# Optimization experiments

Hardware: AMD Instinct MI355X
Metric: run time of the kernel (lower is better)

The kernel has to match this reference:

```python
import jax, jax.numpy as jnp
import numpy as np

N = 50000      # nodes
E = 800000     # edges
F_IN = 512     # num_features
H = 128        # hidden


def setup_inputs() -> dict:
    key = jax.random.key(0)
    ks = jax.random.split(key, 10)
    edge_index = jax.random.randint(ks[0], (2, E), 0, N, dtype=jnp.int64 if jax.config.jax_enable_x64 else jnp.int32)
    x = jax.random.normal(ks[1], (N, F_IN), jnp.float32)
    weights = jax.random.uniform(ks[2], (E,), jnp.float32)
    def w(i, shape, fan):
        return jax.random.normal(ks[i], shape, jnp.float32) / np.sqrt(fan).astype(np.float32)
    return {
        "edge_index": edge_index,
        "x": x,
        "weights": weights,
        "W_lin1": w(3, (F_IN, H), F_IN), "b_lin1": jnp.zeros((H,), jnp.float32),
        "W_conv1": w(4, (H, 2 * H), H), "b_conv1": jnp.zeros((2 * H,), jnp.float32),
        "W_mu": w(5, (2 * H, H), 2 * H), "b_mu": jnp.zeros((H,), jnp.float32),
        "W_lin": w(6, (2 * H, 1), 2 * H), "b_lin": jnp.zeros((1,), jnp.float32),
    }


def gcn_conv(x, W, b, src, dst, ew, n):
    """PyG GCNConv with edge weights: add self-loops (weight 1), symmetric norm, scatter-add."""
    loop = jnp.arange(n, dtype=src.dtype)
    s2 = jnp.concatenate([src, loop])
    d2 = jnp.concatenate([dst, loop])
    w2 = jnp.concatenate([ew, jnp.ones((n,), x.dtype)])
    deg = jax.ops.segment_sum(w2, d2, num_segments=n)          # weighted in-degree incl. self-loop
    dinv = jnp.where(deg > 0, deg, 1.0) ** -0.5
    dinv = jnp.where(deg > 0, dinv, 0.0)
    norm = dinv[s2] * w2 * dinv[d2]                            # [E+N]
    h = x @ W                                                   # [N, out]
    out = jax.ops.segment_sum(h[s2] * norm[:, None], d2, num_segments=n)
    return out + b


def reference(edge_index, x, weights, W_lin1, b_lin1, W_conv1, b_conv1, W_mu, b_mu, W_lin, b_lin):
    n = x.shape[0]
    src, dst = edge_index[0], edge_index[1]
    # eval mode: dropout is identity, VGAE.encode returns mu
    h = x @ W_lin1 + b_lin1                                     # lin1
    h = jax.nn.relu(gcn_conv(h, W_conv1, b_conv1, src, dst, weights, n))
    z = gcn_conv(h, W_mu, b_mu, src, dst, weights, n)           # mu == embeddings
    emb_edges = jnp.concatenate([z[src], z[dst]], axis=1)       # [E, 2H]
    out = jax.nn.sigmoid(emb_edges @ W_lin + b_lin)
    return out.squeeze(-1)                                      # [E]
```

## Files before the change

kernel.cpp:

```cpp
#include <hip/hip_runtime.h>
#include <hip/hip_bf16.h>
#include <math.h>


#define NSL 256
#define RSH 8
#define RNG 256

typedef __attribute__((ext_vector_type(8))) short bf16x8;
typedef __attribute__((ext_vector_type(4))) float f32x4;

typedef const __attribute__((address_space(1))) unsigned int* gas_t;
typedef __attribute__((address_space(3))) unsigned int* las_t;

static __device__ __forceinline__ void gload_lds16(const void* g, void* l) {
    __builtin_amdgcn_global_load_lds((gas_t)g, (las_t)l, 16, 0, 0);
}

static __device__ __forceinline__ ushort f2b(float f) {
    __hip_bfloat16 h = __float2bfloat16(f);
    return *(ushort*)&h;
}
static __device__ __forceinline__ float b2f(ushort u) {
    unsigned int v = ((unsigned int)u) << 16;
    return *(float*)&v;
}
static __device__ __forceinline__ bf16x8 cvt8(float4 a, float4 b) {
    bf16x8 r;
    r[0] = (short)f2b(a.x); r[1] = (short)f2b(a.y); r[2] = (short)f2b(a.z); r[3] = (short)f2b(a.w);
    r[4] = (short)f2b(b.x); r[5] = (short)f2b(b.y); r[6] = (short)f2b(b.z); r[7] = (short)f2b(b.w);
    return r;
}


__global__ __launch_bounds__(256) void bucket_count(const int* __restrict__ dst,
                                                    int* __restrict__ cntA, int E, int NR) {
    __shared__ int lc[256];
    const int b = blockIdx.x, t = threadIdx.x;
    lc[t] = 0;
    __syncthreads();
    const int beg = (int)((long long)b * E / NSL);
    const int end = (int)((long long)(b + 1) * E / NSL);
    for (int e = beg + t; e < end; e += 256) atomicAdd(&lc[dst[e] >> RSH], 1);
    __syncthreads();
    if (t < NR) cntA[b * NR + t] = lc[t];
}

__global__ __launch_bounds__(256) void range_scan(int* __restrict__ cntA,
                                                  int* __restrict__ rtot, int NR) {
    __shared__ int s_[256];
    const int r = blockIdx.x, t = threadIdx.x;
    int v = cntA[t * NR + r];
    s_[t] = v;
    __syncthreads();
    for (int off = 1; off < 256; off <<= 1) {
        int add = (t >= off) ? s_[t - off] : 0;
        __syncthreads();
        s_[t] += add;
        __syncthreads();
    }
    cntA[t * NR + r] = s_[t] - v;
    if (t == 255) rtot[r] = s_[t];
}

__global__ __launch_bounds__(256) void base_scan(const int* __restrict__ rtot,
                                                 int* __restrict__ baseOut, int NR) {
    __shared__ int s_[256];
    const int t = threadIdx.x;
    int v = (t < NR) ? rtot[t] : 0;
    s_[t] = v;
    __syncthreads();
    for (int off = 1; off < 256; off <<= 1) {
        int add = (t >= off) ? s_[t - off] : 0;
        __syncthreads();
        s_[t] += add;
        __syncthreads();
    }
    if (t < NR) baseOut[t] = s_[t] - v;
    if (t == NR - 1) baseOut[NR] = s_[t];
}

__global__ __launch_bounds__(256) void bucket_scatter(const int* __restrict__ src,
                                                      const int* __restrict__ dst,
                                                      const float* __restrict__ w,
                                                      const int* __restrict__ cntA,
                                                      const int* __restrict__ baseOut,
                                                      unsigned int* __restrict__ packB,
                                                      float* __restrict__ wB, int E, int NR) {
    __shared__ int cur[256];
    const int b = blockIdx.x, t = threadIdx.x;
    if (t < NR) cur[t] = cntA[b * NR + t] + baseOut[t];
    __syncthreads();
    const int beg = (int)((long long)b * E / NSL);
    const int end = (int)((long long)(b + 1) * E / NSL);
    for (int e = beg + t; e < end; e += 256) {
        int d = dst[e];
        int r = d >> RSH;
        int pos = atomicAdd(&cur[r], 1);
        packB[pos] = ((unsigned int)(d & (RNG - 1)) << 24) | (unsigned int)src[e];
        wB[pos] = w[e];
    }
}

__global__ __launch_bounds__(256) void range_deg(const unsigned int* __restrict__ packB,
                                                 const float* __restrict__ wB,
                                                 const int* __restrict__ baseOut,
                                                 float* __restrict__ dinv,
                                                 int* __restrict__ offs,
                                                 int N, int E) {
    __shared__ float lw[256];
    __shared__ int lc[256];
    __shared__ int sc[256];
    const int r = blockIdx.x, t = threadIdx.x;
    lw[t] = 0.f; lc[t] = 0;
    __syncthreads();
    const int beg = baseOut[r], end = baseOut[r + 1];
    for (int e = beg + t; e < end; e += 256) {
        unsigned int pk = packB[e];
        int dl = pk >> 24;
        atomicAdd(&lc[dl], 1);
        atomicAdd(&lw[dl], wB[e]);
    }
    __syncthreads();
    int v = lc[t];
    sc[t] = v;
    __syncthreads();
    for (int off = 1; off < 256; off <<= 1) {
        int add = (t >= off) ? sc[t - off] : 0;
        __syncthreads();
        sc[t] += add;
        __syncthreads();
    }
    int node = (r << RSH) + t;
    if (node < N) {
        dinv[node] = 1.0f / sqrtf(1.0f + lw[t]);
        offs[node] = beg + sc[t] - v;
    }
    if (r == 0 && t == 0) offs[N] = E;
}

__global__ __launch_bounds__(256) void csr_build(const unsigned int* __restrict__ packB,
                                                 const float* __restrict__ wB,
                                                 const int* __restrict__ baseOut,
                                                 const float* __restrict__ dinv,
                                                 const int* __restrict__ offs,
                                                 int* __restrict__ es,
                                                 float* __restrict__ en, int N) {
    __shared__ int cur[256];
    __shared__ float ldv[256];
    const int r = blockIdx.x, t = threadIdx.x;
    const int node = (r << RSH) + t;
    cur[t] = (node < N) ? offs[node] : 0;
    ldv[t] = (node < N) ? dinv[node] : 0.f;
    __syncthreads();
    const int beg = baseOut[r], end = baseOut[r + 1];
    for (int e = beg + t; e < end; e += 256) {
        unsigned int pk = packB[e];
        int dl = pk >> 24;
        int s = pk & 0xFFFFFF;
        float nrm = dinv[s] * wB[e] * ldv[dl];
        int pos = atomicAdd(&cur[dl], 1);
        es[pos] = s;
        en[pos] = nrm;
    }
}


__global__ __launch_bounds__(256) void tconv_kernel(const float* __restrict__ B,
                                                    ushort* __restrict__ BT, int K, int Nn) {
    int i = blockIdx.x * 256 + threadIdx.x;
    if (i < K * Nn) {
        int k = i / Nn, n = i % Nn;
        BT[(size_t)n * K + k] = f2b(B[i]);
    }
}

__global__ __launch_bounds__(256) void fold_kernel(const float* __restrict__ Wm,
                                                   const float* __restrict__ Wl,
                                                   const float* __restrict__ bm,
                                                   float* __restrict__ wmp,
                                                   float* __restrict__ wmq,
                                                   float* __restrict__ bpq) {
    int j = threadIdx.x;
    float sp = 0.f, sq = 0.f;
    for (int k = 0; k < 128; ++k) {
        float v = Wm[(size_t)j * 128 + k];
        sp += v * Wl[k];
        sq += v * Wl[128 + k];
    }
    wmp[j] = sp; wmq[j] = sq;
    if (j == 0) { float s = 0.f; for (int k = 0; k < 128; ++k) s += bm[k] * Wl[k];       bpq[0] = s; }
    if (j == 1) { float s = 0.f; for (int k = 0; k < 128; ++k) s += bm[k] * Wl[128 + k]; bpq[1] = s; }
}

__global__ __launch_bounds__(256) void gemm1_mfma(const float* __restrict__ A,
                                                  const ushort* __restrict__ BT,
                                                  const float* __restrict__ bias,
                                                  ushort* __restrict__ C, int M) {
    __shared__ float  As[64 * 64];
    __shared__ ushort Bs[128 * 64];
    char* AsB = (char*)As;
    char* BsB = (char*)Bs;
    const int t = threadIdx.x;
    const int bm = blockIdx.x * 64;
    const int lane = t & 63;
    const int wid = t >> 6;
    const int wm = (wid >> 1) * 32, wn = (wid & 1) * 64;

    f32x4 acc[2][4] = {};

    const int a_row_l = (lane >> 4);
    const int a_ib    = (lane & 15) * 16;
    const int b_row_l = (lane >> 3);
    const int b_ib    = (lane & 7) * 16;

#pragma unroll 1
    for (int tt = 0; tt < 8; ++tt) {
        const int k0 = tt * 64;
#pragma unroll
        for (int j = 0; j < 4; ++j) {
            int c = wid * 4 + j;
            int row = c * 4 + a_row_l;
            int sw = a_ib ^ ((row & 7) << 5);
            int grow = min(bm + row, M - 1);
            const char* src = (const char*)A + ((size_t)grow * 512 + k0) * 4 + sw;
            gload_lds16(src, AsB + c * 1024);
        }
#pragma unroll
        for (int j = 0; j < 4; ++j) {
            int c = wid * 4 + j;
            int row = c * 8 + b_row_l;
            int sw = b_ib ^ ((row & 7) << 4);
            const char* src = (const char*)BT + (size_t)row * 1024 + k0 * 2 + sw;
            gload_lds16(src, BsB + c * 1024);
        }
        __syncthreads();
#pragma unroll
        for (int ks = 0; ks < 2; ++ks) {
            bf16x8 af[2], bfr[4];
#pragma unroll
            for (int mi = 0; mi < 2; ++mi) {
                int r = wm + mi * 16 + (lane & 15);
                int byte = r * 256 + ks * 128 + (lane >> 4) * 32;
                byte ^= (r & 7) << 5;
                float4 f0 = *(const float4*)(AsB + byte);
                float4 f1 = *(const float4*)(AsB + byte + 16);
                af[mi] = cvt8(f0, f1);
            }
#pragma unroll
            for (int ni = 0; ni < 4; ++ni) {
                int r = wn + ni * 16 + (lane & 15);
                int byte = r * 128 + ks * 64 + (lane >> 4) * 16;
                byte ^= (r & 7) << 4;
                bfr[ni] = *(const bf16x8*)(BsB + byte);
            }
#pragma unroll
            for (int mi = 0; mi < 2; ++mi)
#pragma unroll
                for (int ni = 0; ni < 4; ++ni)
                    acc[mi][ni] = __builtin_amdgcn_mfma_f32_16x16x32_bf16(af[mi], bfr[ni], acc[mi][ni], 0, 0, 0);
        }
        __syncthreads();
    }

#pragma unroll
    for (int ni = 0; ni < 4; ++ni) {
        int col = wn + ni * 16 + (lane & 15);
        float bv = bias[col];
#pragma unroll
        for (int mi = 0; mi < 2; ++mi)
#pragma unroll
            for (int r = 0; r < 4; ++r) {
                int row = bm + wm + mi * 16 + (lane >> 4) * 4 + r;
                if (row < M) C[(size_t)row * 128 + col] = f2b(acc[mi][ni][r] + bv);
            }
    }
}

__global__ __launch_bounds__(256) void aggregate_bf16(const ushort* __restrict__ h,
                                                      const int* __restrict__ offs,
                                                      const int* __restrict__ es,
                                                      const float* __restrict__ en,
                                                      const float* __restrict__ dinv,
                                                      ushort* __restrict__ out, int n) {
    int wave = (int)((blockIdx.x * (size_t)blockDim.x + threadIdx.x) >> 6);
    int lane = threadIdx.x & 63;
    if (wave >= n) return;
    float di = dinv[wave];
    float sw = di * di;
    unsigned int hv = *(const unsigned int*)(h + (size_t)wave * 128 + lane * 2);
    float ax = sw * b2f((ushort)(hv & 0xffff));
    float ay = sw * b2f((ushort)(hv >> 16));
    int beg = offs[wave], end = offs[wave + 1];
    for (int e = beg; e < end; e += 8) {
        int sx[8]; float wx[8];
#pragma unroll
        for (int j = 0; j < 8; ++j) {
            bool v = (e + j) < end;
            sx[j] = v ? es[e + j] : wave;
            wx[j] = v ? en[e + j] : 0.f;
        }
        unsigned int vv[8];
#pragma unroll
        for (int j = 0; j < 8; ++j)
            vv[j] = *(const unsigned int*)(h + (size_t)sx[j] * 128 + lane * 2);
#pragma unroll
        for (int j = 0; j < 8; ++j) {
            ax += wx[j] * b2f((ushort)(vv[j] & 0xffff));
            ay += wx[j] * b2f((ushort)(vv[j] >> 16));
        }
    }
    unsigned int o = (unsigned int)f2b(ax) | ((unsigned int)f2b(ay) << 16);
    *(unsigned int*)(out + (size_t)wave * 128 + lane * 2) = o;
}

__global__ __launch_bounds__(64) void gemm2_stream(const ushort* __restrict__ A,
                                                   const ushort* __restrict__ BT,
                                                   const float* __restrict__ bc,
                                                   const float* __restrict__ wmp,
                                                   const float* __restrict__ wmq,
                                                   float* __restrict__ pe,
                                                   float* __restrict__ qe, int M) {
    const int lane = threadIdx.x;
    const int r0 = blockIdx.x * 16;
    const int lrow = lane & 15;
    const int lk   = (lane >> 4) * 8;

    f32x4 acc[16] = {};

    const ushort* a  = A  + (size_t)min(r0 + lrow, M - 1) * 128 + lk;
    const ushort* bp = BT + (size_t)lrow * 128 + lk;

#pragma unroll
    for (int ks = 0; ks < 4; ++ks) {
        const int k0 = ks * 32;
        bf16x8 af = *(const bf16x8*)(a + k0);
#pragma unroll
        for (int ni = 0; ni < 16; ++ni) {
            bf16x8 bfr = *(const bf16x8*)(bp + (size_t)ni * 16 * 128 + k0);
            acc[ni] = __builtin_amdgcn_mfma_f32_16x16x32_bf16(af, bfr, acc[ni], 0, 0, 0);
        }
    }

    float bcv[16], wpv[16], wqv[16];
#pragma unroll
    for (int ni = 0; ni < 16; ++ni) {
        int col = ni * 16 + lrow;
        bcv[ni] = bc[col];
        wpv[ni] = wmp[col];
        wqv[ni] = wmq[col];
    }
#pragma unroll
    for (int r = 0; r < 4; ++r) {
        float sp = 0.f, sq = 0.f;
#pragma unroll
        for (int ni = 0; ni < 16; ++ni) {
            float h = fmaxf(acc[ni][r] + bcv[ni], 0.f);
            sp += h * wpv[ni];
            sq += h * wqv[ni];
        }
#pragma unroll
        for (int off = 1; off < 16; off <<= 1) {
            sp += __shfl_xor(sp, off);
            sq += __shfl_xor(sq, off);
        }
        if (lrow == 0) {
            int row = r0 + (lane >> 4) * 4 + r;
            if (row < M) { pe[row] = sp; qe[row] = sq; }
        }
    }
}

__global__ __launch_bounds__(256) void agg_scalar(const float* __restrict__ pe,
                                                  const float* __restrict__ qe,
                                                  const int* __restrict__ offs,
                                                  const int* __restrict__ es,
                                                  const float* __restrict__ en,
                                                  const float* __restrict__ dinv,
                                                  const float* __restrict__ bpq,
                                                  float* __restrict__ p,
                                                  float* __restrict__ q, int n) {
    int i = blockIdx.x * 256 + threadIdx.x;
    if (i >= n) return;
    float di = dinv[i];
    float sw = di * di;
    float ap = sw * pe[i], aq = sw * qe[i];
    int beg = offs[i], end = offs[i + 1];
    for (int k = beg; k < end; k += 4) {
        int sx[4]; float wx[4];
#pragma unroll
        for (int j = 0; j < 4; ++j) {
            bool v = (k + j) < end;
            sx[j] = v ? es[k + j] : i;
            wx[j] = v ? en[k + j] : 0.f;
        }
        float pv[4], qv[4];
#pragma unroll
        for (int j = 0; j < 4; ++j) { pv[j] = pe[sx[j]]; qv[j] = qe[sx[j]]; }
#pragma unroll
        for (int j = 0; j < 4; ++j) { ap += wx[j] * pv[j]; aq += wx[j] * qv[j]; }
    }
    p[i] = ap + bpq[0];
    q[i] = aq + bpq[1];
}

__global__ __launch_bounds__(256) void edge_out_kernel(const int* __restrict__ src,
                                                       const int* __restrict__ dst,
                                                       const float* __restrict__ p,
                                                       const float* __restrict__ q,
                                                       const float* __restrict__ bl,
                                                       float* __restrict__ out, int e) {
    int i = blockIdx.x * 256 + threadIdx.x;
    if (i < e) {
        float t = p[src[i]] + q[dst[i]] + bl[0];
        out[i] = 1.0f / (1.0f + expf(-t));
    }
}


extern "C" void kernel_launch(void* const* d_in, const int* in_sizes, int n_in,
                              void* d_out, int out_size, void* d_ws, size_t ws_size,
                              hipStream_t stream) {
    const int*   edge_index = (const int*)d_in[0];
    const float* x   = (const float*)d_in[1];
    const float* w   = (const float*)d_in[2];
    const float* W1  = (const float*)d_in[3];
    const float* b1  = (const float*)d_in[4];
    const float* Wc  = (const float*)d_in[5];
    const float* bc  = (const float*)d_in[6];
    const float* Wm  = (const float*)d_in[7];
    const float* bm  = (const float*)d_in[8];
    const float* Wl  = (const float*)d_in[9];
    const float* bl  = (const float*)d_in[10];
    float* out = (float*)d_out;

    const int E  = in_sizes[2];
    const int H  = in_sizes[4];
    const int F  = in_sizes[3] / H;
    const int N  = in_sizes[1] / F;
    const int H2 = 2 * H;
    const int NR = (N + RNG - 1) / RNG;

    const int* src = edge_index;
    const int* dst = edge_index + E;

    char* ws = (char*)d_ws;
    size_t off = 0;
    auto alloc = [&](size_t bytes) -> void* {
        off = (off + 255) & ~(size_t)255;
        void* r = ws + off;
        off += bytes;
        return r;
    };
    int*          cntA    = (int*)         alloc((size_t)NSL * NR * 4);
    int*          rtot    = (int*)         alloc((size_t)NR * 4);
    int*          baseOut = (int*)         alloc((size_t)(NR + 1) * 4);
    unsigned int* packB   = (unsigned int*)alloc((size_t)E * 4);
    float*        wB      = (float*)       alloc((size_t)E * 4);
    float*        dinv    = (float*)       alloc((size_t)N * 4);
    int*          offs    = (int*)         alloc((size_t)(N + 1) * 4);
    int*          es      = (int*)         alloc((size_t)E * 4);
    float*        en      = (float*)       alloc((size_t)E * 4);
    ushort*       h0_bf   = (ushort*)      alloc((size_t)N * H * 2);
    ushort*       agg1_bf = (ushort*)      alloc((size_t)N * H * 2);
    ushort*       W1T     = (ushort*)      alloc((size_t)H * F * 2);
    ushort*       WcT     = (ushort*)      alloc((size_t)H2 * H * 2);
    float*        wmp     = (float*)       alloc(H2 * 4);
    float*        wmq     = (float*)       alloc(H2 * 4);
    float*        bpq     = (float*)       alloc(2 * 4);
    float*        pe      = (float*)       alloc((size_t)N * 4);
    float*        qe      = (float*)       alloc((size_t)N * 4);
    float*        p       = (float*)       alloc((size_t)N * 4);
    float*        q       = (float*)       alloc((size_t)N * 4);
    (void)ws_size; (void)n_in; (void)out_size;

    int nbN  = (N + 255) / 256;
    int nbE  = (E + 255) / 256;
    int nbW  = (int)(((size_t)N * 64 + 255) / 256);
    int nb64 = (N + 63) / 64;
    int nb16 = (N + 15) / 16;

    bucket_count<<<NSL, 256, 0, stream>>>(dst, cntA, E, NR);
    range_scan<<<NR, 256, 0, stream>>>(cntA, rtot, NR);
    base_scan<<<1, 256, 0, stream>>>(rtot, baseOut, NR);
    bucket_scatter<<<NSL, 256, 0, stream>>>(src, dst, w, cntA, baseOut, packB, wB, E, NR);
    range_deg<<<NR, 256, 0, stream>>>(packB, wB, baseOut, dinv, offs, N, E);
    csr_build<<<NR, 256, 0, stream>>>(packB, wB, baseOut, dinv, offs, es, en, N);

    tconv_kernel<<<(F * H + 255) / 256, 256, 0, stream>>>(W1, W1T, F, H);
    tconv_kernel<<<(H * H2 + 255) / 256, 256, 0, stream>>>(Wc, WcT, H, H2);
    fold_kernel<<<1, 256, 0, stream>>>(Wm, Wl, bm, wmp, wmq, bpq);

    gemm1_mfma<<<nb64, 256, 0, stream>>>(x, W1T, b1, h0_bf, N);
    aggregate_bf16<<<nbW, 256, 0, stream>>>(h0_bf, offs, es, en, dinv, agg1_bf, N);
    gemm2_stream<<<nb16, 64, 0, stream>>>(agg1_bf, WcT, bc, wmp, wmq, pe, qe, N);
    agg_scalar<<<nbN, 256, 0, stream>>>(pe, qe, offs, es, en, dinv, bpq, p, q, N);
    edge_out_kernel<<<nbE, 256, 0, stream>>>(src, dst, p, q, bl, out, E);
}
```

Measured before the change: 184.2 us.

## Fuse degree and CSR build, interleave edge records, prescale by dinv, double-buffer GEMM1

The degree and CSR-build kernels are merged into one range_build kernel. Edge source and weight are packed into interleaved uint2 records, so each edge needs one load instead of two. Symmetric normalization is refactored: dinv is applied to rows in the GEMM epilogue and to destinations after aggregation, so the per-edge dinv[src] gather and multiply go away. GEMM1 now double-buffers its LDS tiles with global_load_lds prefetch and manual vmcnt waits to overlap loads with MFMA, at the cost of twice the LDS per block.

Measured after the change: 197.7 us. +7.3%, slower.

```diff
diff --git a/kernel.cpp b/kernel.cpp
--- a/kernel.cpp
+++ b/kernel.cpp
@@ -85,8 +85,7 @@
                                                       const float* __restrict__ w,
                                                       const int* __restrict__ cntA,
                                                       const int* __restrict__ baseOut,
-                                                      unsigned int* __restrict__ packB,
-                                                      float* __restrict__ wB, int E, int NR) {
+                                                      uint2* __restrict__ rec, int E, int NR) {
     __shared__ int cur[256];
     const int b = blockIdx.x, t = threadIdx.x;
     if (t < NR) cur[t] = cntA[b * NR + t] + baseOut[t];
@@ -97,17 +96,17 @@
         int d = dst[e];
         int r = d >> RSH;
         int pos = atomicAdd(&cur[r], 1);
-        packB[pos] = ((unsigned int)(d & (RNG - 1)) << 24) | (unsigned int)src[e];
-        wB[pos] = w[e];
-    }
-}
-
-__global__ __launch_bounds__(256) void range_deg(const unsigned int* __restrict__ packB,
-                                                 const float* __restrict__ wB,
-                                                 const int* __restrict__ baseOut,
-                                                 float* __restrict__ dinv,
-                                                 int* __restrict__ offs,
-                                                 int N, int E) {
+        rec[pos] = make_uint2(((unsigned int)(d & (RNG - 1)) << 24) | (unsigned int)src[e],
+                              __float_as_uint(w[e]));
+    }
+}
+
+__global__ __launch_bounds__(256) void range_build(const uint2* __restrict__ rec,
+                                                   const int* __restrict__ baseOut,
+                                                   float* __restrict__ dinv,
+                                                   int* __restrict__ offs,
+                                                   uint2* __restrict__ ce,
+                                                   int N, int E) {
     __shared__ float lw[256];
     __shared__ int lc[256];
     __shared__ int sc[256];
@@ -116,10 +115,10 @@
     __syncthreads();
     const int beg = baseOut[r], end = baseOut[r + 1];
     for (int e = beg + t; e < end; e += 256) {
-        unsigned int pk = packB[e];
-        int dl = pk >> 24;
+        uint2 pk = rec[e];
+        int dl = pk.x >> 24;
         atomicAdd(&lc[dl], 1);
-        atomicAdd(&lw[dl], wB[e]);
+        atomicAdd(&lw[dl], __uint_as_float(pk.y));
     }
     __syncthreads();
     int v = lc[t];
@@ -131,37 +130,20 @@
         sc[t] += add;
         __syncthreads();
     }
-    int node = (r << RSH) + t;
+    const int node = (r << RSH) + t;
+    const int o = beg + sc[t] - v;
     if (node < N) {
         dinv[node] = 1.0f / sqrtf(1.0f + lw[t]);
-        offs[node] = beg + sc[t] - v;
+        offs[node] = o;
     }
     if (r == 0 && t == 0) offs[N] = E;
-}
-
-__global__ __launch_bounds__(256) void csr_build(const unsigned int* __restrict__ packB,
-                                                 const float* __restrict__ wB,
-                                                 const int* __restrict__ baseOut,
-                                                 const float* __restrict__ dinv,
-                                                 const int* __restrict__ offs,
-                                                 int* __restrict__ es,
-                                                 float* __restrict__ en, int N) {
-    __shared__ int cur[256];
-    __shared__ float ldv[256];
-    const int r = blockIdx.x, t = threadIdx.x;
-    const int node = (r << RSH) + t;
-    cur[t] = (node < N) ? offs[node] : 0;
-    ldv[t] = (node < N) ? dinv[node] : 0.f;
-    __syncthreads();
-    const int beg = baseOut[r], end = baseOut[r + 1];
+    lc[t] = o;
+    __syncthreads();
     for (int e = beg + t; e < end; e += 256) {
-        unsigned int pk = packB[e];
-        int dl = pk >> 24;
-        int s = pk & 0xFFFFFF;
-        float nrm = dinv[s] * wB[e] * ldv[dl];
-        int pos = atomicAdd(&cur[dl], 1);
-        es[pos] = s;
-        en[pos] = nrm;
+        uint2 pk = rec[e];
+        int dl = pk.x >> 24;
+        int pos = atomicAdd(&lc[dl], 1);
+        ce[pos] = make_uint2(pk.x & 0xFFFFFF, pk.y);
     }
 }
 
@@ -196,11 +178,10 @@
 __global__ __launch_bounds__(256) void gemm1_mfma(const float* __restrict__ A,
                                                   const ushort* __restrict__ BT,
                                                   const float* __restrict__ bias,
+                                                  const float* __restrict__ dinv,
                                                   ushort* __restrict__ C, int M) {
-    __shared__ float  As[64 * 64];
-    __shared__ ushort Bs[128 * 64];
-    char* AsB = (char*)As;
-    char* BsB = (char*)Bs;
+    __shared__ float  As[2][64 * 64];
+    __shared__ ushort Bs[2][128 * 64];
     const int t = threadIdx.x;
     const int bm = blockIdx.x * 64;
     const int lane = t & 63;
@@ -214,9 +195,7 @@
     const int b_row_l = (lane >> 3);
     const int b_ib    = (lane & 7) * 16;
 
-#pragma unroll 1
-    for (int tt = 0; tt < 8; ++tt) {
-        const int k0 = tt * 64;
+    auto stage = [&](int buf, int k0) {
 #pragma unroll
         for (int j = 0; j < 4; ++j) {
             int c = wid * 4 + j;
@@ -224,7 +203,7 @@
             int sw = a_ib ^ ((row & 7) << 5);
             int grow = min(bm + row, M - 1);
             const char* src = (const char*)A + ((size_t)grow * 512 + k0) * 4 + sw;
-            gload_lds16(src, AsB + c * 1024);
+            gload_lds16(src, (char*)As[buf] + c * 1024);
         }
 #pragma unroll
         for (int j = 0; j < 4; ++j) {
@@ -232,9 +211,24 @@
             int row = c * 8 + b_row_l;
             int sw = b_ib ^ ((row & 7) << 4);
             const char* src = (const char*)BT + (size_t)row * 1024 + k0 * 2 + sw;
-            gload_lds16(src, BsB + c * 1024);
-        }
-        __syncthreads();
+            gload_lds16(src, (char*)Bs[buf] + c * 1024);
+        }
+    };
+
+    stage(0, 0);
+    int cur = 0;
+#pragma unroll 1
+    for (int tt = 0; tt < 8; ++tt) {
+        if (tt < 7) {
+            stage(cur ^ 1, (tt + 1) * 64);
+            asm volatile("s_waitcnt vmcnt(8)" ::: "memory");
+        } else {
+            asm volatile("s_waitcnt vmcnt(0)" ::: "memory");
+        }
+        __builtin_amdgcn_sched_barrier(0);
+        __builtin_amdgcn_s_barrier();
+        const char* AsB = (const char*)As[cur];
+        const char* BsB = (const char*)Bs[cur];
 #pragma unroll
         for (int ks = 0; ks < 2; ++ks) {
             bf16x8 af[2], bfr[4];
@@ -260,58 +254,59 @@
                 for (int ni = 0; ni < 4; ++ni)
                     acc[mi][ni] = __builtin_amdgcn_mfma_f32_16x16x32_bf16(af[mi], bfr[ni], acc[mi][ni], 0, 0, 0);
         }
-        __syncthreads();
-    }
-
-#pragma unroll
-    for (int ni = 0; ni < 4; ++ni) {
-        int col = wn + ni * 16 + (lane & 15);
-        float bv = bias[col];
-#pragma unroll
-        for (int mi = 0; mi < 2; ++mi)
-#pragma unroll
-            for (int r = 0; r < 4; ++r) {
-                int row = bm + wm + mi * 16 + (lane >> 4) * 4 + r;
-                if (row < M) C[(size_t)row * 128 + col] = f2b(acc[mi][ni][r] + bv);
+        __builtin_amdgcn_s_barrier();
+        cur ^= 1;
+    }
+
+#pragma unroll
+    for (int mi = 0; mi < 2; ++mi)
+#pragma unroll
+        for (int r = 0; r < 4; ++r) {
+            int row = bm + wm + mi * 16 + (lane >> 4) * 4 + r;
+            if (row < M) {
+                float dv = dinv[row];
+#pragma unroll
+                for (int ni = 0; ni < 4; ++ni) {
+                    int col = wn + ni * 16 + (lane & 15);
+                    C[(size_t)row * 128 + col] = f2b((acc[mi][ni][r] + bias[col]) * dv);
+                }
             }
-    }
-}
-
-__global__ __launch_bounds__(256) void aggregate_bf16(const ushort* __restrict__ h,
+        }
+}
+
+__global__ __launch_bounds__(256) void aggregate_bf16(const ushort* __restrict__ hs,
                                                       const int* __restrict__ offs,
-                                                      const int* __restrict__ es,
-                                                      const float* __restrict__ en,
+                                                      const uint2* __restrict__ ce,
                                                       const float* __restrict__ dinv,
                                                       ushort* __restrict__ out, int n) {
-    int wave = (int)((blockIdx.x * (size_t)blockDim.x + threadIdx.x) >> 6);
+    int node = (int)((blockIdx.x * (size_t)blockDim.x + threadIdx.x) >> 6);
     int lane = threadIdx.x & 63;
-    if (wave >= n) return;
-    float di = dinv[wave];
-    float sw = di * di;
-    unsigned int hv = *(const unsigned int*)(h + (size_t)wave * 128 + lane * 2);
-    float ax = sw * b2f((ushort)(hv & 0xffff));
-    float ay = sw * b2f((ushort)(hv >> 16));
-    int beg = offs[wave], end = offs[wave + 1];
+    if (node >= n) return;
+    unsigned int hv = *(const unsigned int*)(hs + (size_t)node * 128 + lane * 2);
+    float ax = b2f((ushort)(hv & 0xffff));
+    float ay = b2f((ushort)(hv >> 16));
+    int beg = offs[node], end = offs[node + 1];
     for (int e = beg; e < end; e += 8) {
-        int sx[8]; float wx[8];
+        uint2 rr[8];
 #pragma unroll
         for (int j = 0; j < 8; ++j) {
             bool v = (e + j) < end;
-            sx[j] = v ? es[e + j] : wave;
-            wx[j] = v ? en[e + j] : 0.f;
+            rr[j] = v ? ce[e + j] : make_uint2((unsigned)node, 0u);
         }
         unsigned int vv[8];
 #pragma unroll
         for (int j = 0; j < 8; ++j)
-            vv[j] = *(const unsigned int*)(h + (size_t)sx[j] * 128 + lane * 2);
+            vv[j] = *(const unsigned int*)(hs + (size_t)rr[j].x * 128 + lane * 2);
 #pragma unroll
         for (int j = 0; j < 8; ++j) {
-            ax += wx[j] * b2f((ushort)(vv[j] & 0xffff));
-            ay += wx[j] * b2f((ushort)(vv[j] >> 16));
-        }
-    }
-    unsigned int o = (unsigned int)f2b(ax) | ((unsigned int)f2b(ay) << 16);
-    *(unsigned int*)(out + (size_t)wave * 128 + lane * 2) = o;
+            float wj = __uint_as_float(rr[j].y);
+            ax += wj * b2f((ushort)(vv[j] & 0xffff));
+            ay += wj * b2f((ushort)(vv[j] >> 16));
+        }
+    }
+    float dv = dinv[node];
+    unsigned int o = (unsigned int)f2b(ax * dv) | ((unsigned int)f2b(ay * dv) << 16);
+    *(unsigned int*)(out + (size_t)node * 128 + lane * 2) = o;
 }
 
 __global__ __launch_bounds__(64) void gemm2_stream(const ushort* __restrict__ A,
@@ -319,6 +314,7 @@
                                                    const float* __restrict__ bc,
                                                    const float* __restrict__ wmp,
                                                    const float* __restrict__ wmq,
+                                                   const float* __restrict__ dinv,
                                                    float* __restrict__ pe,
                                                    float* __restrict__ qe, int M) {
     const int lane = threadIdx.x;
@@ -366,7 +362,11 @@
         }
         if (lrow == 0) {
             int row = r0 + (lane >> 4) * 4 + r;
-            if (row < M) { pe[row] = sp; qe[row] = sq; }
+            if (row < M) {
+                float dv = dinv[row];
+                pe[row] = sp * dv;
+                qe[row] = sq * dv;
+            }
         }
     }
 }
@@ -374,34 +374,35 @@
 __global__ __launch_bounds__(256) void agg_scalar(const float* __restrict__ pe,
                                                   const float* __restrict__ qe,
                                                   const int* __restrict__ offs,
-                                                  const int* __restrict__ es,
-                                                  const float* __restrict__ en,
+                                                  const uint2* __restrict__ ce,
                                                   const float* __restrict__ dinv,
                                                   const float* __restrict__ bpq,
                                                   float* __restrict__ p,
                                                   float* __restrict__ q, int n) {
     int i = blockIdx.x * 256 + threadIdx.x;
     if (i >= n) return;
-    float di = dinv[i];
-    float sw = di * di;
-    float ap = sw * pe[i], aq = sw * qe[i];
+    float ap = pe[i], aq = qe[i];
     int beg = offs[i], end = offs[i + 1];
     for (int k = beg; k < end; k += 4) {
-        int sx[4]; float wx[4];
+        uint2 rr[4];
 #pragma unroll
         for (int j = 0; j < 4; ++j) {
             bool v = (k + j) < end;
-            sx[j] = v ? es[k + j] : i;
-            wx[j] = v ? en[k + j] : 0.f;
+            rr[j] = v ? ce[k + j] : make_uint2((unsigned)i, 0u);
         }
         float pv[4], qv[4];
 #pragma unroll
-        for (int j = 0; j < 4; ++j) { pv[j] = pe[sx[j]]; qv[j] = qe[sx[j]]; }
-#pragma unroll
-        for (int j = 0; j < 4; ++j) { ap += wx[j] * pv[j]; aq += wx[j] * qv[j]; }
-    }
-    p[i] = ap + bpq[0];
-    q[i] = aq + bpq[1];
+        for (int j = 0; j < 4; ++j) { pv[j] = pe[rr[j].x]; qv[j] = qe[rr[j].x]; }
+#pragma unroll
+        for (int j = 0; j < 4; ++j) {
+            float wj = __uint_as_float(rr[j].y);
+            ap += wj * pv[j];
+            aq += wj * qv[j];
+        }
+    }
+    float dv = dinv[i];
+    p[i] = ap * dv + bpq[0];
+    q[i] = aq * dv + bpq[1];
 }
 
 __global__ __launch_bounds__(256) void edge_out_kernel(const int* __restrict__ src,
@@ -452,26 +453,24 @@
         off += bytes;
         return r;
     };
-    int*          cntA    = (int*)         alloc((size_t)NSL * NR * 4);
-    int*          rtot    = (int*)         alloc((size_t)NR * 4);
-    int*          baseOut = (int*)         alloc((size_t)(NR + 1) * 4);
-    unsigned int* packB   = (unsigned int*)alloc((size_t)E * 4);
-    float*        wB      = (float*)       alloc((size_t)E * 4);
-    float*        dinv    = (float*)       alloc((size_t)N * 4);
-    int*          offs    = (int*)         alloc((size_t)(N + 1) * 4);
-    int*          es      = (int*)         alloc((size_t)E * 4);
-    float*        en      = (float*)       alloc((size_t)E * 4);
-    ushort*       h0_bf   = (ushort*)      alloc((size_t)N * H * 2);
-    ushort*       agg1_bf = (ushort*)      alloc((size_t)N * H * 2);
-    ushort*       W1T     = (ushort*)      alloc((size_t)H * F * 2);
-    ushort*       WcT     = (ushort*)      alloc((size_t)H2 * H * 2);
-    float*        wmp     = (float*)       alloc(H2 * 4);
-    float*        wmq     = (float*)       alloc(H2 * 4);
-    float*        bpq     = (float*)       alloc(2 * 4);
-    float*        pe      = (float*)       alloc((size_t)N * 4);
-    float*        qe      = (float*)       alloc((size_t)N * 4);
-    float*        p       = (float*)       alloc((size_t)N * 4);
-    float*        q       = (float*)       alloc((size_t)N * 4);
+    int*    cntA    = (int*)   alloc((size_t)NSL * NR * 4);
+    int*    rtot    = (int*)   alloc((size_t)NR * 4);
+    int*    baseOut = (int*)   alloc((size_t)(NR + 1) * 4);
+    uint2*  rec     = (uint2*) alloc((size_t)E * 8);
+    uint2*  ce      = (uint2*) alloc((size_t)E * 8);
+    float*  dinv    = (float*) alloc((size_t)N * 4);
+    int*    offs    = (int*)   alloc((size_t)(N + 1) * 4);
+    ushort* hs_bf   = (ushort*)alloc((size_t)N * H * 2);
+    ushort* agg1_bf = (ushort*)alloc((size_t)N * H * 2);
+    ushort* W1T     = (ushort*)alloc((size_t)H * F * 2);
+    ushort* WcT     = (ushort*)alloc((size_t)H2 * H * 2);
+    float*  wmp     = (float*) alloc(H2 * 4);
+    float*  wmq     = (float*) alloc(H2 * 4);
+    float*  bpq     = (float*) alloc(2 * 4);
+    float*  pe      = (float*) alloc((size_t)N * 4);
+    float*  qe      = (float*) alloc((size_t)N * 4);
+    float*  p       = (float*) alloc((size_t)N * 4);
+    float*  q       = (float*) alloc((size_t)N * 4);
     (void)ws_size; (void)n_in; (void)out_size;
 
     int nbN  = (N + 255) / 256;
@@ -483,17 +482,16 @@
     bucket_count<<<NSL, 256, 0, stream>>>(dst, cntA, E, NR);
     range_scan<<<NR, 256, 0, stream>>>(cntA, rtot, NR);
     base_scan<<<1, 256, 0, stream>>>(rtot, baseOut, NR);
-    bucket_scatter<<<NSL, 256, 0, stream>>>(src, dst, w, cntA, baseOut, packB, wB, E, NR);
-    range_deg<<<NR, 256, 0, stream>>>(packB, wB, baseOut, dinv, offs, N, E);
-    csr_build<<<NR, 256, 0, stream>>>(packB, wB, baseOut, dinv, offs, es, en, N);
+    bucket_scatter<<<NSL, 256, 0, stream>>>(src, dst, w, cntA, baseOut, rec, E, NR);
+    range_build<<<NR, 256, 0, stream>>>(rec, baseOut, dinv, offs, ce, N, E);
 
     tconv_kernel<<<(F * H + 255) / 256, 256, 0, stream>>>(W1, W1T, F, H);
     tconv_kernel<<<(H * H2 + 255) / 256, 256, 0, stream>>>(Wc, WcT, H, H2);
     fold_kernel<<<1, 256, 0, stream>>>(Wm, Wl, bm, wmp, wmq, bpq);
 
-    gemm1_mfma<<<nb64, 256, 0, stream>>>(x, W1T, b1, h0_bf, N);
-    aggregate_bf16<<<nbW, 256, 0, stream>>>(h0_bf, offs, es, en, dinv, agg1_bf, N);
-    gemm2_stream<<<nb16, 64, 0, stream>>>(agg1_bf, WcT, bc, wmp, wmq, pe, qe, N);
-    agg_scalar<<<nbN, 256, 0, stream>>>(pe, qe, offs, es, en, dinv, bpq, p, q, N);
+    gemm1_mfma<<<nb64, 256, 0, stream>>>(x, W1T, b1, dinv, hs_bf, N);
+    aggregate_bf16<<<nbW, 256, 0, stream>>>(hs_bf, offs, ce, dinv, agg1_bf, N);
+    gemm2_stream<<<nb16, 64, 0, stream>>>(agg1_bf, WcT, bc, wmp, wmq, dinv, pe, qe, N);
+    agg_scalar<<<nbN, 256, 0, stream>>>(pe, qe, offs, ce, dinv, bpq, p, q, N);
     edge_out_kernel<<<nbE, 256, 0, stream>>>(src, dst, p, q, bl, out, E);
 }
```
